# Performance work log

Measured on AMD Instinct MI355X. Metric: run time of the kernel, lower is better.

Reference implementation:

```python
import jax, jax.numpy as jnp
from jax import lax
import numpy as np

B, T, D, H = 64, 512, 1024, 1024

def _lstm_layer(x_tbd, mask_tb, W, U, b):
    """Keras-style LSTM over time-major x (T,B,D). Gate order i,f,g,o.
    Masked timesteps carry previous h,c (Keras mask semantics)."""
    Bsz = x_tbd.shape[1]
    Hsz = U.shape[0]
    # precompute input projection once: (T,B,4H)
    xz = jnp.einsum('tbd,dh->tbh', x_tbd, W) + b

    def step(carry, inp):
        h, c = carry
        zx, m = inp
        z = zx + h @ U
        i, f, g, o = jnp.split(z, 4, axis=-1)
        i = jax.nn.sigmoid(i)
        f = jax.nn.sigmoid(f)
        g = jnp.tanh(g)
        o = jax.nn.sigmoid(o)
        c_new = f * c + i * g
        h_new = o * jnp.tanh(c_new)
        m = m[:, None]
        h2 = jnp.where(m, h_new, h)
        c2 = jnp.where(m, c_new, c)
        return (h2, c2), h2

    h0 = jnp.zeros((Bsz, Hsz), x_tbd.dtype)
    c0 = jnp.zeros((Bsz, Hsz), x_tbd.dtype)
    (h, c), hs = lax.scan(step, (h0, c0), (xz, mask_tb))
    return hs, h, c


def setup_inputs() -> dict:
    key = jax.random.key(0)
    ks = jax.random.split(key, 8)
    sD = 1.0 / np.sqrt(D)
    sH = 1.0 / np.sqrt(H)
    x = jax.random.normal(ks[0], (B, T, D), dtype=jnp.float32)
    lengths = jax.random.randint(ks[1], (B,), 1, T + 1, dtype=jnp.int32)
    # Keras unit_forget_bias: bias zeros except forget gate slice = 1
    b = jnp.zeros((4 * H,), jnp.float32).at[H:2 * H].set(1.0)
    return {
        'x': x,
        'lengths': lengths,
        'W0': jax.random.normal(ks[2], (D, 4 * H), dtype=jnp.float32) * sD,
        'U0': jax.random.normal(ks[3], (H, 4 * H), dtype=jnp.float32) * sH,
        'b0': b,
        'W1': jax.random.normal(ks[4], (H, 4 * H), dtype=jnp.float32) * sH,
        'U1': jax.random.normal(ks[5], (H, 4 * H), dtype=jnp.float32) * sH,
        'b1': b,
    }


def reference(x, lengths, W0, U0, b0, W1, U1, b1):
    Tlen = x.shape[1]
    mask = jnp.arange(Tlen)[None, :] < lengths[:, None]  # (B,T)
    mask_tb = mask.T  # (T,B)
    x_tbd = jnp.transpose(x, (1, 0, 2))  # time-major
    out0, _, _ = _lstm_layer(x_tbd, mask_tb, W0, U0, b0)
    out1, h, c = _lstm_layer(out0, mask_tb, W1, U1, b1)
    rnnout = jnp.transpose(out1, (1, 0, 2))  # (B,T,H)
    return rnnout, h, c
```

## Files before the change

kernel.cpp:

```cpp
#include <hip/hip_runtime.h>
#include <hip/hip_bf16.h>


#define NTT 512

typedef __attribute__((ext_vector_type(8))) short short8;
typedef __attribute__((ext_vector_type(4))) float floatx4;
typedef __attribute__((ext_vector_type(4))) unsigned short ushort4v;
typedef unsigned long long ull;

#define LDS_TOTAL 90112

#define AT_LD(p) __hip_atomic_load((p), __ATOMIC_RELAXED, __HIP_MEMORY_SCOPE_AGENT)
#define AT_ST(p, v) __hip_atomic_store((p), (v), __ATOMIC_RELAXED, __HIP_MEMORY_SCOPE_AGENT)
#define AT_ADD(p, v) __hip_atomic_fetch_add((p), (v), __ATOMIC_RELAXED, __HIP_MEMORY_SCOPE_AGENT)

__device__ __forceinline__ unsigned short f2bf(float f) {
  unsigned int u = __float_as_uint(f);
  u += 0x7fffu + ((u >> 16) & 1u);
  return (unsigned short)(u >> 16);
}
__device__ __forceinline__ float sigmf(float x) { return 1.0f / (1.0f + __expf(-x)); }
__device__ __forceinline__ float tanhfa(float x) { return 1.0f - 2.0f / (1.0f + __expf(2.0f * x)); }

__device__ __forceinline__ void fullbar(ull* fb) {
  __syncthreads();
  if (threadIdx.x == 0) {
    __builtin_amdgcn_fence(__ATOMIC_RELEASE, "agent");
    AT_ADD(fb, 1ull);
    while (AT_LD(fb) < 256ull) __builtin_amdgcn_s_sleep(1);
    __builtin_amdgcn_fence(__ATOMIC_ACQUIRE, "agent");
  }
  __syncthreads();
}

__device__ __forceinline__ short8 ldfrag(const char* p) { return *(const short8*)p; }
__device__ __forceinline__ short8 ldcoh(const char* p) {
  union { short8 s; ull q[2]; } u;
  u.q[0] = AT_LD((const ull*)p);
  u.q[1] = AT_LD((const ull*)(p + 8));
  return u.s;
}

__device__ __forceinline__ void ringfill(const char* const* aPm, short8 (*af)[4]) {
#pragma unroll
  for (int kt = 0; kt < 8; ++kt)
#pragma unroll
    for (int mt = 0; mt < 4; ++mt) af[kt][mt] = ldfrag(aPm[mt] + kt * 64);
}

__device__ __forceinline__ void kmain(const char* const* aPm, short8 (*af)[4],
                                      const short8 (*bfr)[2], floatx4 (*acc)[2]) {
#pragma unroll
  for (int kt = 0; kt < 16; ++kt) {
#pragma unroll
    for (int mt = 0; mt < 4; ++mt)
#pragma unroll
      for (int nt = 0; nt < 2; ++nt)
        acc[mt][nt] = __builtin_amdgcn_mfma_f32_16x16x32_bf16(
            af[kt & 7][mt], bfr[kt][nt], acc[mt][nt], 0, 0, 0);
    if (kt < 8) {
#pragma unroll
      for (int mt = 0; mt < 4; ++mt)
        af[kt & 7][mt] = ldfrag(aPm[mt] + (kt + 8) * 64);
    }
  }
}

__device__ __forceinline__ void ringchunk(const char* const* aPm, short8 (*afc)[4], int kb) {
#pragma unroll
  for (int j = 0; j < 4; ++j)
#pragma unroll
    for (int mt = 0; mt < 4; ++mt) afc[j][mt] = ldcoh(aPm[mt] + (kb + j) * 64);
}

__device__ __forceinline__ void kchunk(const short8 (*afc)[4], const short8 (*bfr)[2],
                                       floatx4 (*acc)[2], int kb) {
#pragma unroll
  for (int j = 0; j < 4; ++j)
#pragma unroll
    for (int mt = 0; mt < 4; ++mt)
#pragma unroll
      for (int nt = 0; nt < 2; ++nt)
        acc[mt][nt] = __builtin_amdgcn_mfma_f32_16x16x32_bf16(
            afc[j][mt], bfr[kb + j][nt], acc[mt][nt], 0, 0, 0);
}

__global__ __launch_bounds__(256, 1) void lstm2_persist(
    const float* __restrict__ xin, const int* __restrict__ lens,
    const float* __restrict__ W0, const float* __restrict__ U0, const float* __restrict__ b0v,
    const float* __restrict__ W1, const float* __restrict__ U1, const float* __restrict__ b1v,
    float* __restrict__ out, ull* __restrict__ ws) {
  extern __shared__ char smem[];
  float* red = (float*)smem;

  unsigned* flags0 = (unsigned*)(ws + 16);
  unsigned* flags1 = (unsigned*)(ws + 80);
  ull* fbar = ws + 1024;
  unsigned short* hbufs = (unsigned short*)(ws + 2048);

  const int tid = threadIdx.x;
  const int bid = blockIdx.x;
  const int layer = bid >> 7;
  const int sub = bid & 127;
  const int hc0 = sub * 8;
  const int wave = tid >> 6;
  const int lane = tid & 63;
  const int c16 = lane & 15;
  const int rowgrp = lane >> 4;
  unsigned* flagsL = layer ? flags1 : flags0;

  unsigned short* h0r[4] = {hbufs, hbufs + 65536, hbufs + 131072, hbufs + 196608};
  unsigned short* h1r[2] = {hbufs + 262144, hbufs + 327680};

  const unsigned int gid = (unsigned int)bid * 256u + (unsigned int)tid;
  for (unsigned int i = gid; i < 196608u; i += 65536u) ((unsigned int*)hbufs)[i] = 0u;
  {
    const floatx4* xs = (const floatx4*)xin;
    for (unsigned int q = gid; q < 8388608u; q += 65536u) {
      unsigned int d4 = q & 255u;
      unsigned int bt = q >> 8;
      floatx4 v = xs[q];
      ushort4v o;
      o.x = f2bf(v.x); o.y = f2bf(v.y); o.z = f2bf(v.z); o.w = f2bf(v.w);
      *((ushort4v*)((char*)out + (size_t)bt * 4096) + d4) = o;
    }
  }
  const float* Wm = layer ? W1 : W0;
  const float* Um = layer ? U1 : U0;
  const float* Bsrc = (wave < 2) ? Wm : Um;
  const int kbase = (wave & 1) * 512;
  short8 bf[16][2];
#pragma unroll
  for (int kt = 0; kt < 16; ++kt)
#pragma unroll
    for (int nt = 0; nt < 2; ++nt) {
      const int zc = (nt * 2 + (c16 >> 3)) * 1024 + hc0 + (c16 & 7);
      const float* col = Bsrc + (size_t)(kbase + kt * 32 + rowgrp * 8) * 4096 + zc;
      short8 v;
#pragma unroll
      for (int j = 0; j < 8; ++j) v[j] = (short)f2bf(col[(size_t)j * 4096]);
      bf[kt][nt] = v;
    }
  const float* bv = layer ? b1v : b0v;
  const float bias0 = bv[(c16 >> 3) * 1024 + hc0 + (c16 & 7)];
  const float bias1 = bv[(2 + (c16 >> 3)) * 1024 + hc0 + (c16 & 7)];
  int lens4[4];
#pragma unroll
  for (int r = 0; r < 4; ++r) lens4[r] = lens[wave * 16 + rowgrp * 4 + r];

  fullbar(fbar);

  float hst[4] = {0.f, 0.f, 0.f, 0.f};
  float cst[4] = {0.f, 0.f, 0.f, 0.f};
  const int col = hc0 + c16;

#pragma unroll 1
  for (int t = 0; t < NTT; ++t) {
    const char* aPm[4];
    short8 af[8][4];
    bool isX;
    {
      const char* base0;
      size_t pitch;
      if (layer == 0) {
        if (wave < 2) { base0 = (const char*)out + (size_t)t * 4096 + (size_t)wave * 1024;
                        pitch = (size_t)NTT * 4096; isX = true; }
        else          { base0 = (const char*)h0r[(t + 3) & 3] + (size_t)(wave - 2) * 1024;
                        pitch = 2048; isX = false; }
      } else {
        if (wave < 2) { base0 = (const char*)h0r[t & 3] + (size_t)wave * 1024; }
        else          { base0 = (const char*)h1r[(t + 1) & 1] + (size_t)(wave - 2) * 1024; }
        pitch = 2048; isX = false;
      }
      const char* aP = base0 + (size_t)c16 * pitch + (size_t)rowgrp * 16;
#pragma unroll
      for (int mt = 0; mt < 4; ++mt) aPm[mt] = aP + (size_t)mt * 16 * pitch;
    }

    floatx4 acc[4][2];
#pragma unroll
    for (int mt = 0; mt < 4; ++mt)
#pragma unroll
      for (int nt = 0; nt < 2; ++nt) { floatx4 z = {0.f, 0.f, 0.f, 0.f}; acc[mt][nt] = z; }

    if (isX) {
      ringfill(aPm, af);
      kmain(aPm, af, bf, acc);
    } else {
      if (layer == 0 && t >= 4) {
        const unsigned g4 = (unsigned)(t - 3);
        while (true) {
          bool ok = (AT_LD(flags1 + lane) >= g4) && (AT_LD(flags1 + 64 + lane) >= g4);
          if (__all(ok)) break;
          __builtin_amdgcn_s_sleep(2);
        }
      }
      const unsigned* fl;
      int half;
      unsigned tgt;
      if (layer == 0)      { fl = flags0; half = wave - 2; tgt = (unsigned)t; }
      else if (wave < 2)   { fl = flags0; half = wave;     tgt = (unsigned)(t + 1); }
      else                 { fl = flags1; half = wave - 2; tgt = (unsigned)t; }
      const unsigned* fb = fl + half * 64;

      ull rdy = __ballot(AT_LD(fb + lane) >= tgt);
#pragma unroll
      for (int g = 0; g < 4; ++g) {
        const ull need = 0xFFFFull << (16 * g);
        while ((rdy & need) != need) {
          __builtin_amdgcn_s_sleep(1);
          rdy = __ballot(AT_LD(fb + lane) >= tgt);
        }
        ringchunk(aPm, &af[(g & 1) * 4], g * 4);
        if (g) kchunk(&af[((g - 1) & 1) * 4], bf, acc, (g - 1) * 4);
      }
      kchunk(&af[4], bf, acc, 12);
    }

#pragma unroll
    for (int mt = 0; mt < 4; ++mt)
      if (mt != wave) {
        int slot = mt * 3 + wave - (wave > mt ? 1 : 0);
        *(floatx4*)&red[((slot * 2 + 0) * 64 + lane) * 4] = acc[mt][0];
        *(floatx4*)&red[((slot * 2 + 1) * 64 + lane) * 4] = acc[mt][1];
      }
    __syncthreads();
    floatx4 z0 = acc[wave][0], z1 = acc[wave][1];
#pragma unroll
    for (int q = 0; q < 3; ++q) {
      int slot = wave * 3 + q;
      z0 += *(const floatx4*)&red[((slot * 2 + 0) * 64 + lane) * 4];
      z1 += *(const floatx4*)&red[((slot * 2 + 1) * 64 + lane) * 4];
    }
    z0 += bias0;
    z1 += bias1;

    unsigned short* hW = layer ? h1r[t & 1] : h0r[t & 3];
    float2 f2s[4];

#pragma unroll
    for (int r = 0; r < 4; ++r) {
      float zi = z0[r], zg = z1[r];
      float zf = __shfl_xor(zi, 8);
      float zo = __shfl_xor(zg, 8);
      float h2, hu_f = 0.f;
      unsigned short hu = 0;
      if (c16 < 8) {
        float ig = sigmf(zi), fg = sigmf(zf), gg = tanhfa(zg), og = sigmf(zo);
        float cn = fg * cst[r] + ig * gg;
        float hn = og * tanhfa(cn);
        bool m = t < lens4[r];
        h2 = m ? hn : hst[r];
        float c2 = m ? cn : cst[r];
        hst[r] = h2;
        cst[r] = c2;
        hu = f2bf(h2);
        hu_f = h2;
      }
      unsigned int up = __shfl_xor((unsigned int)hu, 1);
      float hp = __shfl_xor(hu_f, 1);
      if (c16 < 8 && !(c16 & 1)) {
        int b = wave * 16 + rowgrp * 4 + r;
        unsigned int w = (unsigned int)hu | (up << 16);
        AT_ST((unsigned int*)(hW + b * 1024 + col), w);
        f2s[r] = make_float2(hu_f, hp);
      }
    }

    asm volatile("s_waitcnt vmcnt(0)" ::: "memory");
    __syncthreads();
    if (tid == 0) AT_ST(flagsL + sub, (unsigned)(t + 1));

    if (layer && c16 < 8 && !(c16 & 1)) {
#pragma unroll
      for (int r = 0; r < 4; ++r) {
        int b = wave * 16 + rowgrp * 4 + r;
        *(float2*)&out[((size_t)b * 512 + (size_t)t) * 1024 + col] = f2s[r];
      }
    }
  }

  if (layer && c16 < 8) {
#pragma unroll
    for (int r = 0; r < 4; ++r) {
      int b = wave * 16 + rowgrp * 4 + r;
      out[(size_t)33554432 + (size_t)b * 1024 + col] = hst[r];
      out[(size_t)33554432 + 65536 + (size_t)b * 1024 + col] = cst[r];
    }
  }
}

extern "C" void kernel_launch(void* const* d_in, const int* in_sizes, int n_in,
                              void* d_out, int out_size, void* d_ws, size_t ws_size,
                              hipStream_t stream) {
  (void)in_sizes; (void)n_in; (void)out_size; (void)ws_size;
  const float* x  = (const float*)d_in[0];
  const int* lens = (const int*)d_in[1];
  const float* W0 = (const float*)d_in[2];
  const float* U0 = (const float*)d_in[3];
  const float* b0 = (const float*)d_in[4];
  const float* W1 = (const float*)d_in[5];
  const float* U1 = (const float*)d_in[6];
  const float* b1 = (const float*)d_in[7];

  (void)hipFuncSetAttribute((const void*)lstm2_persist,
                            hipFuncAttributeMaxDynamicSharedMemorySize, LDS_TOTAL);
  hipMemsetAsync(d_ws, 0, 16384, stream);

  lstm2_persist<<<dim3(256), dim3(256), LDS_TOTAL, stream>>>(
      x, lens, W0, U0, b0, W1, U1, b1, (float*)d_out, (ull*)d_ws);
}
```

Measured before the change: 10.23 ms.

## Store hidden state in per-block contiguous tiles and wait once per step

```diff
diff --git a/kernel.cpp b/kernel.cpp
--- a/kernel.cpp
+++ b/kernel.cpp
@@ -42,15 +42,14 @@
   return u.s;
 }
 
-__device__ __forceinline__ void ringfill(const char* const* aPm, short8 (*af)[4]) {
+__device__ __forceinline__ void ringfillX(const char* const* aPm, short8 (*af)[4]) {
 #pragma unroll
   for (int kt = 0; kt < 8; ++kt)
 #pragma unroll
     for (int mt = 0; mt < 4; ++mt) af[kt][mt] = ldfrag(aPm[mt] + kt * 64);
 }
-
-__device__ __forceinline__ void kmain(const char* const* aPm, short8 (*af)[4],
-                                      const short8 (*bfr)[2], floatx4 (*acc)[2]) {
+__device__ __forceinline__ void kmainX(const char* const* aPm, short8 (*af)[4],
+                                       const short8 (*bfr)[2], floatx4 (*acc)[2]) {
 #pragma unroll
   for (int kt = 0; kt < 16; ++kt) {
 #pragma unroll
@@ -67,23 +66,28 @@
   }
 }
 
-__device__ __forceinline__ void ringchunk(const char* const* aPm, short8 (*afc)[4], int kb) {
-#pragma unroll
-  for (int j = 0; j < 4; ++j)
-#pragma unroll
-    for (int mt = 0; mt < 4; ++mt) afc[j][mt] = ldcoh(aPm[mt] + (kb + j) * 64);
-}
-
-__device__ __forceinline__ void kchunk(const short8 (*afc)[4], const short8 (*bfr)[2],
-                                       floatx4 (*acc)[2], int kb) {
-#pragma unroll
-  for (int j = 0; j < 4; ++j)
+__device__ __forceinline__ void ringfillH(const char* const* aPm, short8 (*af)[4]) {
+#pragma unroll
+  for (int kt = 0; kt < 8; ++kt)
+#pragma unroll
+    for (int mt = 0; mt < 4; ++mt) af[kt][mt] = ldcoh(aPm[mt] + kt * 4096);
+}
+__device__ __forceinline__ void kmainH(const char* const* aPm, short8 (*af)[4],
+                                       const short8 (*bfr)[2], floatx4 (*acc)[2]) {
+#pragma unroll
+  for (int kt = 0; kt < 16; ++kt) {
 #pragma unroll
     for (int mt = 0; mt < 4; ++mt)
 #pragma unroll
       for (int nt = 0; nt < 2; ++nt)
         acc[mt][nt] = __builtin_amdgcn_mfma_f32_16x16x32_bf16(
-            afc[j][mt], bfr[kb + j][nt], acc[mt][nt], 0, 0, 0);
+            af[kt & 7][mt], bfr[kt][nt], acc[mt][nt], 0, 0, 0);
+    if (kt < 8) {
+#pragma unroll
+      for (int mt = 0; mt < 4; ++mt)
+        af[kt & 7][mt] = ldcoh(aPm[mt] + (kt + 8) * 4096);
+    }
+  }
 }
 
 __global__ __launch_bounds__(256, 1) void lstm2_persist(
@@ -93,6 +97,7 @@
     float* __restrict__ out, ull* __restrict__ ws) {
   extern __shared__ char smem[];
   float* red = (float*)smem;
+  unsigned short* hstage = (unsigned short*)(smem + 24576);
 
   unsigned* flags0 = (unsigned*)(ws + 16);
   unsigned* flags1 = (unsigned*)(ws + 80);
@@ -159,35 +164,32 @@
   for (int t = 0; t < NTT; ++t) {
     const char* aPm[4];
     short8 af[8][4];
-    bool isX;
-    {
-      const char* base0;
-      size_t pitch;
-      if (layer == 0) {
-        if (wave < 2) { base0 = (const char*)out + (size_t)t * 4096 + (size_t)wave * 1024;
-                        pitch = (size_t)NTT * 4096; isX = true; }
-        else          { base0 = (const char*)h0r[(t + 3) & 3] + (size_t)(wave - 2) * 1024;
-                        pitch = 2048; isX = false; }
-      } else {
-        if (wave < 2) { base0 = (const char*)h0r[t & 3] + (size_t)wave * 1024; }
-        else          { base0 = (const char*)h1r[(t + 1) & 1] + (size_t)(wave - 2) * 1024; }
-        pitch = 2048; isX = false;
-      }
+    floatx4 acc[4][2];
+#pragma unroll
+    for (int mt = 0; mt < 4; ++mt)
+#pragma unroll
+      for (int nt = 0; nt < 2; ++nt) { floatx4 z = {0.f, 0.f, 0.f, 0.f}; acc[mt][nt] = z; }
+
+    if (layer == 0 && wave < 2) {
+      const char* base0 = (const char*)out + (size_t)t * 4096 + (size_t)wave * 1024;
+      const size_t pitch = (size_t)NTT * 4096;
       const char* aP = base0 + (size_t)c16 * pitch + (size_t)rowgrp * 16;
 #pragma unroll
       for (int mt = 0; mt < 4; ++mt) aPm[mt] = aP + (size_t)mt * 16 * pitch;
-    }
-
-    floatx4 acc[4][2];
-#pragma unroll
-    for (int mt = 0; mt < 4; ++mt)
-#pragma unroll
-      for (int nt = 0; nt < 2; ++nt) { floatx4 z = {0.f, 0.f, 0.f, 0.f}; acc[mt][nt] = z; }
-
-    if (isX) {
-      ringfill(aPm, af);
-      kmain(aPm, af, bf, acc);
+      ringfillX(aPm, af);
+      kmainX(aPm, af, bf, acc);
     } else {
+      const char* hb;
+      int khalf;
+      const unsigned* fl;
+      unsigned tgt;
+      if (layer == 0)    { hb = (const char*)h0r[(t + 3) & 3]; khalf = wave - 2; fl = flags0; tgt = (unsigned)t; }
+      else if (wave < 2) { hb = (const char*)h0r[t & 3];       khalf = wave;     fl = flags0; tgt = (unsigned)(t + 1); }
+      else               { hb = (const char*)h1r[(t + 1) & 1]; khalf = wave - 2; fl = flags1; tgt = (unsigned)t; }
+#pragma unroll
+      for (int mt = 0; mt < 4; ++mt)
+        aPm[mt] = hb + (size_t)khalf * 65536 + (size_t)rowgrp * 1024 + (size_t)(mt * 16 + c16) * 16;
+
       if (layer == 0 && t >= 4) {
         const unsigned g4 = (unsigned)(t - 3);
         while (true) {
@@ -196,26 +198,11 @@
           __builtin_amdgcn_s_sleep(2);
         }
       }
-      const unsigned* fl;
-      int half;
-      unsigned tgt;
-      if (layer == 0)      { fl = flags0; half = wave - 2; tgt = (unsigned)t; }
-      else if (wave < 2)   { fl = flags0; half = wave;     tgt = (unsigned)(t + 1); }
-      else                 { fl = flags1; half = wave - 2; tgt = (unsigned)t; }
-      const unsigned* fb = fl + half * 64;
-
-      ull rdy = __ballot(AT_LD(fb + lane) >= tgt);
-#pragma unroll
-      for (int g = 0; g < 4; ++g) {
-        const ull need = 0xFFFFull << (16 * g);
-        while ((rdy & need) != need) {
-          __builtin_amdgcn_s_sleep(1);
-          rdy = __ballot(AT_LD(fb + lane) >= tgt);
-        }
-        ringchunk(aPm, &af[(g & 1) * 4], g * 4);
-        if (g) kchunk(&af[((g - 1) & 1) * 4], bf, acc, (g - 1) * 4);
-      }
-      kchunk(&af[4], bf, acc, 12);
+      const unsigned* fb = fl + khalf * 64;
+      while (!__all(AT_LD(fb + lane) >= tgt)) __builtin_amdgcn_s_sleep(1);
+
+      ringfillH(aPm, af);
+      kmainH(aPm, af, bf, acc);
     }
 
 #pragma unroll
@@ -244,33 +231,35 @@
       float zi = z0[r], zg = z1[r];
       float zf = __shfl_xor(zi, 8);
       float zo = __shfl_xor(zg, 8);
-      float h2, hu_f = 0.f;
+      float hu_f = 0.f;
       unsigned short hu = 0;
       if (c16 < 8) {
         float ig = sigmf(zi), fg = sigmf(zf), gg = tanhfa(zg), og = sigmf(zo);
         float cn = fg * cst[r] + ig * gg;
         float hn = og * tanhfa(cn);
         bool m = t < lens4[r];
-        h2 = m ? hn : hst[r];
+        float h2 = m ? hn : hst[r];
         float c2 = m ? cn : cst[r];
         hst[r] = h2;
         cst[r] = c2;
         hu = f2bf(h2);
         hu_f = h2;
+        hstage[(wave * 16 + rowgrp * 4 + r) * 8 + c16] = hu;
       }
-      unsigned int up = __shfl_xor((unsigned int)hu, 1);
       float hp = __shfl_xor(hu_f, 1);
-      if (c16 < 8 && !(c16 & 1)) {
-        int b = wave * 16 + rowgrp * 4 + r;
-        unsigned int w = (unsigned int)hu | (up << 16);
-        AT_ST((unsigned int*)(hW + b * 1024 + col), w);
-        f2s[r] = make_float2(hu_f, hp);
-      }
-    }
-
-    asm volatile("s_waitcnt vmcnt(0)" ::: "memory");
+      if (c16 < 8 && !(c16 & 1)) f2s[r] = make_float2(hu_f, hp);
+    }
+
     __syncthreads();
-    if (tid == 0) AT_ST(flagsL + sub, (unsigned)(t + 1));
+    if (wave == 0) {
+      const ull* hs = (const ull*)hstage;
+      ull q0 = hs[2 * lane], q1 = hs[2 * lane + 1];
+      char* dst = (char*)hW + (size_t)sub * 1024 + (size_t)lane * 16;
+      AT_ST((ull*)dst, q0);
+      AT_ST((ull*)(dst + 8), q1);
+      asm volatile("s_waitcnt vmcnt(0)" ::: "memory");
+      if (lane == 0) AT_ST(flagsL + sub, (unsigned)(t + 1));
+    }
 
     if (layer && c16 < 8 && !(c16 & 1)) {
 #pragma unroll
```

Result: faster. 8.747 ms (-14.5%).
